# Performance work log

Measured on AMD Instinct MI355X. Metric: run time of the kernel, lower is better.

Reference implementation:

```python
import jax, jax.numpy as jnp
import numpy as np
import math

B, T, D, H = 4, 2048, 1024, 16
DH = D // H


def setup_inputs() -> dict:
    key = jax.random.key(0)
    k1, k2, k3 = jax.random.split(key, 3)
    x = jax.random.normal(k1, (B, T, D), dtype=jnp.float32)
    # causal mask: True = masked (positions j > i)
    attn_mask = jnp.triu(jnp.ones((T, T), dtype=bool), k=1)
    key_padding_mask = jnp.zeros((B, T), dtype=bool)  # no padding
    W_qkv = jax.random.normal(k2, (D, 3 * D), dtype=jnp.float32) / math.sqrt(D)
    W_out = jax.random.normal(k3, (D, D), dtype=jnp.float32) / math.sqrt(D)
    return {"x": x, "W_qkv": W_qkv, "W_out": W_out,
            "attn_mask": attn_mask, "key_padding_mask": key_padding_mask}


def reference(x, W_qkv, W_out, attn_mask, key_padding_mask):
    # qkv projection (bias=False)
    qkv = x @ W_qkv                                   # [B,T,3D]
    q, k, v = jnp.split(qkv, 3, axis=-1)              # each [B,T,D]
    # reshape to heads: [B,H,T,DH]
    q = q.reshape(B, T, H, DH).transpose(0, 2, 1, 3)
    k = k.reshape(B, T, H, DH).transpose(0, 2, 1, 3)
    v = v.reshape(B, T, H, DH).transpose(0, 2, 1, 3)
    scale = 1.0 / math.sqrt(DH)
    scores = jnp.einsum('bhqd,bhkd->bhqk', q, k) * scale   # [B,H,T,T]
    neg_inf = jnp.float32(-jnp.inf)
    scores = jnp.where(attn_mask[None, None, :, :], neg_inf, scores)
    scores = jnp.where(key_padding_mask[:, None, None, :], neg_inf, scores)
    attn = jax.nn.softmax(scores, axis=-1)            # dropout p=0.0 -> identity
    out = jnp.einsum('bhqk,bhkd->bhqd', attn, v)      # [B,H,T,DH]
    out = out.transpose(0, 2, 1, 3).reshape(B, T, D)
    return out @ W_out
```

## Files before the change

### kernel.cpp

```cpp
#include <hip/hip_runtime.h>
#include <hip/hip_bf16.h>

#define Bsz 4
#define T 2048
#define D 1024
#define H 16
#define DH 64

typedef unsigned short u16;
typedef __attribute__((ext_vector_type(8))) __bf16 bf16x8;
typedef __attribute__((ext_vector_type(4))) float f32x4;

__device__ inline u16 f2bf(float f) {
  union { float f; unsigned u; } v; v.f = f;
  unsigned r = (v.u + 0x7FFFu + ((v.u >> 16) & 1u)) >> 16;
  return (u16)r;
}
__device__ inline unsigned pack_bf16(float a, float b) {
  union { float f; unsigned u; } A, B; A.f = a; B.f = b;
  unsigned au = A.u + 0x8000u, bu = B.u + 0x8000u;
  return __builtin_amdgcn_perm(bu, au, 0x07060302);
}

__device__ inline void gll16(const u16* g, u16* l) {
  __builtin_amdgcn_global_load_lds((const __attribute__((address_space(1))) void*)g,
                                   (__attribute__((address_space(3))) void*)l, 16, 0, 0);
}

__global__ __launch_bounds__(256) void convert_f32_bf16(const float* __restrict__ in,
                                                        u16* __restrict__ out, int n4) {
  int i = blockIdx.x * 256 + threadIdx.x;
  if (i < n4) {
    float4 v = reinterpret_cast<const float4*>(in)[i];
    ushort4 o;
    o.x = f2bf(v.x); o.y = f2bf(v.y); o.z = f2bf(v.z); o.w = f2bf(v.w);
    reinterpret_cast<ushort4*>(out)[i] = o;
  }
}

__global__ __launch_bounds__(256) void transpose_f32_bf16(const float* __restrict__ in,
                                                          u16* __restrict__ out, int K, int N) {
  __shared__ float tile[32][33];
  int tx = threadIdx.x & 31, ty = threadIdx.x >> 5;
  int n0 = blockIdx.x * 32, k0 = blockIdx.y * 32;
  #pragma unroll
  for (int i = 0; i < 4; ++i)
    tile[ty + i * 8][tx] = in[(size_t)(k0 + ty + i * 8) * N + n0 + tx];
  __syncthreads();
  #pragma unroll
  for (int i = 0; i < 4; ++i)
    out[(size_t)(n0 + ty + i * 8) * K + k0 + tx] = f2bf(tile[tx][ty + i * 8]);
}

template <int MODE>
__global__ __launch_bounds__(512, 2) void gemm256(const u16* __restrict__ A, const u16* __restrict__ BT,
                                                  float* __restrict__ C,
                                                  u16* __restrict__ Qh, u16* __restrict__ Kh,
                                                  u16* __restrict__ VTh, int M, int N, int K) {
  __shared__ alignas(16) u16 SA[2][256][64];
  __shared__ alignas(16) u16 SB[2][256][64];
  int tid = threadIdx.x;

  int flat = blockIdx.y * gridDim.x + blockIdx.x;
  int cpx = (int)(gridDim.x * gridDim.y) >> 3;
  int nf = (flat & 7) * cpx + (flat >> 3);
  int bx = nf % (int)gridDim.x, by = nf / (int)gridDim.x;
  int m0 = by * 256, n0 = bx * 256;

  int w = tid >> 6, lane = tid & 63;
  int llo = lane & 15, lhi = lane >> 4;
  int wr = w >> 2, wc = w & 3;

  int cs0 = ((lhi ^ (llo & 7)) << 3);
  int cs1 = (((4 + lhi) ^ (llo & 7)) << 3);

  int srcCol = (((lane & 7) ^ ((lane >> 3) & 7)) << 3);
  const u16* gAl = A + (size_t)(m0 + w * 8 + (lane >> 3)) * K + srcCol;
  const u16* gBl = BT + (size_t)(n0 + w * 8 + (lane >> 3)) * K + srcCol;

  f32x4 acc[8][4];
  #pragma unroll
  for (int i = 0; i < 8; ++i)
    #pragma unroll
    for (int j = 0; j < 4; ++j) acc[i][j] = (f32x4){0.f, 0.f, 0.f, 0.f};

  int nt = K >> 6;

  auto stA = [&](int buf, int h, int c, int kt) {
    gll16(gAl + (h * 128 + c * 64) * K + kt * 64, &SA[buf][h * 128 + c * 64 + w * 8][0]);
  };
  auto stB = [&](int buf, int h, int c, int kt) {
    gll16(gBl + (h * 128 + c * 64) * K + kt * 64, &SB[buf][h * 128 + c * 64 + w * 8][0]);
  };

  stA(0, 0, 0, 0); stA(0, 0, 1, 0); stA(0, 1, 0, 0); stA(0, 1, 1, 0);
  stB(0, 0, 0, 0); stB(0, 0, 1, 0); stB(0, 1, 0, 0); stB(0, 1, 1, 0);
  stB(1, 0, 0, 1); stB(1, 0, 1, 1);
  stA(1, 0, 0, 1); stA(1, 0, 1, 1);
  asm volatile("s_waitcnt vmcnt(4)" ::: "memory");
  __builtin_amdgcn_s_barrier();
  __builtin_amdgcn_sched_barrier(0);

  bf16x8 aA[4][2], bB[4][2];

  #pragma unroll 2
  for (int t = 0; t < nt; ++t) {
    int p = t & 1;

    #pragma unroll
    for (int i = 0; i < 4; ++i) {
      aA[i][0] = *reinterpret_cast<const bf16x8*>(&SA[p][wr * 128 + i * 16 + llo][cs0]);
      aA[i][1] = *reinterpret_cast<const bf16x8*>(&SA[p][wr * 128 + i * 16 + llo][cs1]);
    }
    #pragma unroll
    for (int j = 0; j < 2; ++j) {
      bB[j][0] = *reinterpret_cast<const bf16x8*>(&SB[p][wc * 64 + j * 16 + llo][cs0]);
      bB[j][1] = *reinterpret_cast<const bf16x8*>(&SB[p][wc * 64 + j * 16 + llo][cs1]);
    }
    if (t + 1 < nt) { stA(1 - p, 1, 0, t + 1); stA(1 - p, 1, 1, t + 1); }
    __builtin_amdgcn_s_barrier();
    asm volatile("s_waitcnt lgkmcnt(0)" ::: "memory");
    __builtin_amdgcn_sched_barrier(0);
    __builtin_amdgcn_s_setprio(1);
    #pragma unroll
    for (int i = 0; i < 4; ++i)
      #pragma unroll
      for (int j = 0; j < 2; ++j) {
        acc[i][j] = __builtin_amdgcn_mfma_f32_16x16x32_bf16(aA[i][0], bB[j][0], acc[i][j], 0, 0, 0);
        acc[i][j] = __builtin_amdgcn_mfma_f32_16x16x32_bf16(aA[i][1], bB[j][1], acc[i][j], 0, 0, 0);
      }
    __builtin_amdgcn_s_setprio(0);
    __builtin_amdgcn_s_barrier();
    __builtin_amdgcn_sched_barrier(0);

    #pragma unroll
    for (int j = 2; j < 4; ++j) {
      bB[j][0] = *reinterpret_cast<const bf16x8*>(&SB[p][wc * 64 + j * 16 + llo][cs0]);
      bB[j][1] = *reinterpret_cast<const bf16x8*>(&SB[p][wc * 64 + j * 16 + llo][cs1]);
    }
    if (t + 1 < nt) { stB(1 - p, 1, 0, t + 1); stB(1 - p, 1, 1, t + 1); }
    __builtin_amdgcn_s_barrier();
    asm volatile("s_waitcnt lgkmcnt(0)" ::: "memory");
    __builtin_amdgcn_sched_barrier(0);
    __builtin_amdgcn_s_setprio(1);
    #pragma unroll
    for (int i = 0; i < 4; ++i)
      #pragma unroll
      for (int j = 2; j < 4; ++j) {
        acc[i][j] = __builtin_amdgcn_mfma_f32_16x16x32_bf16(aA[i][0], bB[j][0], acc[i][j], 0, 0, 0);
        acc[i][j] = __builtin_amdgcn_mfma_f32_16x16x32_bf16(aA[i][1], bB[j][1], acc[i][j], 0, 0, 0);
      }
    __builtin_amdgcn_s_setprio(0);
    __builtin_amdgcn_s_barrier();
    __builtin_amdgcn_sched_barrier(0);

    #pragma unroll
    for (int i = 0; i < 4; ++i) {
      aA[i][0] = *reinterpret_cast<const bf16x8*>(&SA[p][wr * 128 + 64 + i * 16 + llo][cs0]);
      aA[i][1] = *reinterpret_cast<const bf16x8*>(&SA[p][wr * 128 + 64 + i * 16 + llo][cs1]);
    }
    if (t + 2 < nt) { stB(p, 0, 0, t + 2); stB(p, 0, 1, t + 2); }
    __builtin_amdgcn_s_barrier();
    asm volatile("s_waitcnt lgkmcnt(0)" ::: "memory");
    __builtin_amdgcn_sched_barrier(0);
    __builtin_amdgcn_s_setprio(1);
    #pragma unroll
    for (int i = 0; i < 4; ++i)
      #pragma unroll
      for (int j = 0; j < 2; ++j) {
        acc[4 + i][j] = __builtin_amdgcn_mfma_f32_16x16x32_bf16(aA[i][0], bB[j][0], acc[4 + i][j], 0, 0, 0);
        acc[4 + i][j] = __builtin_amdgcn_mfma_f32_16x16x32_bf16(aA[i][1], bB[j][1], acc[4 + i][j], 0, 0, 0);
      }
    __builtin_amdgcn_s_setprio(0);
    __builtin_amdgcn_s_barrier();
    __builtin_amdgcn_sched_barrier(0);

    if (t + 2 < nt) { stA(p, 0, 0, t + 2); stA(p, 0, 1, t + 2); }
    __builtin_amdgcn_s_setprio(1);
    #pragma unroll
    for (int i = 0; i < 4; ++i)
      #pragma unroll
      for (int j = 2; j < 4; ++j) {
        acc[4 + i][j] = __builtin_amdgcn_mfma_f32_16x16x32_bf16(aA[i][0], bB[j][0], acc[4 + i][j], 0, 0, 0);
        acc[4 + i][j] = __builtin_amdgcn_mfma_f32_16x16x32_bf16(aA[i][1], bB[j][1], acc[4 + i][j], 0, 0, 0);
      }
    __builtin_amdgcn_s_setprio(0);
    if (t + 2 < nt)      asm volatile("s_waitcnt vmcnt(4)" ::: "memory");
    else if (t + 1 < nt) asm volatile("s_waitcnt vmcnt(0)" ::: "memory");
    __builtin_amdgcn_s_barrier();
    __builtin_amdgcn_sched_barrier(0);
  }

  if (MODE == 0) {
    #pragma unroll
    for (int i = 0; i < 8; ++i) {
      int ml = m0 + wr * 128 + i * 16 + lhi * 4;
      #pragma unroll
      for (int j = 0; j < 4; ++j) {
        int nl = n0 + wc * 64 + j * 16 + llo;
        #pragma unroll
        for (int r = 0; r < 4; ++r)
          C[(size_t)(ml + r) * N + nl] = acc[i][j][r];
      }
    }
  } else {
    int seg = n0 >> 10;
    #pragma unroll
    for (int i = 0; i < 8; ++i) {
      int mbase = m0 + wr * 128 + i * 16 + lhi * 4;
      int t0 = mbase & (T - 1);
      int b_ = mbase >> 11;
      #pragma unroll
      for (int j = 0; j < 4; ++j) {
        int nl = n0 + wc * 64 + j * 16 + llo;
        int h = (nl >> 6) & 15, d = nl & 63;
        int bh = b_ * H + h;
        if (seg == 0) {
          #pragma unroll
          for (int r = 0; r < 4; ++r)
            Qh[((size_t)bh * T + t0 + r) * DH + d] = f2bf(acc[i][j][r] * 0.125f);
        } else if (seg == 1) {
          #pragma unroll
          for (int r = 0; r < 4; ++r)
            Kh[((size_t)bh * T + t0 + r) * DH + d] = f2bf(acc[i][j][r]);
        } else {
          uint2 p;
          p.x = pack_bf16(acc[i][j][0], acc[i][j][1]);
          p.y = pack_bf16(acc[i][j][2], acc[i][j][3]);
          *reinterpret_cast<uint2*>(&VTh[((size_t)bh * DH + d) * T + t0]) = p;
        }
      }
    }
  }
}

template <int MODE>
__global__ __launch_bounds__(256) void gemm128(const u16* __restrict__ A, const u16* __restrict__ BT,
                                               float* __restrict__ C,
                                               u16* __restrict__ Qh, u16* __restrict__ Kh,
                                               u16* __restrict__ VTh, int M, int N, int K) {
  __shared__ u16 As[128][32];
  __shared__ u16 Bs[128][32];
  int tid = threadIdx.x;
  int m0 = blockIdx.y * 128, n0 = blockIdx.x * 128;
  int w = tid >> 6, lane = tid & 63;
  int llo = lane & 15, lhi = lane >> 4;
  int wm = (w >> 1) * 64, wn = (w & 1) * 64;

  f32x4 acc[4][4];
  #pragma unroll
  for (int i = 0; i < 4; ++i)
    #pragma unroll
    for (int j = 0; j < 4; ++j) acc[i][j] = (f32x4){0.f, 0.f, 0.f, 0.f};

  const u16* gA = A + (size_t)(m0 + w * 32 + (lane >> 2)) * K + (lane & 3) * 8;
  const u16* gB = BT + (size_t)(n0 + w * 32 + (lane >> 2)) * K + (lane & 3) * 8;

  for (int k0 = 0; k0 < K; k0 += 32) {
    gll16(gA + k0, &As[w * 32][0]);
    gll16(gA + (size_t)16 * K + k0, &As[w * 32 + 16][0]);
    gll16(gB + k0, &Bs[w * 32][0]);
    gll16(gB + (size_t)16 * K + k0, &Bs[w * 32 + 16][0]);
    __syncthreads();
    bf16x8 af[4], bfr[4];
    #pragma unroll
    for (int i = 0; i < 4; ++i)
      af[i] = *reinterpret_cast<const bf16x8*>(&As[wm + i * 16 + llo][lhi * 8]);
    #pragma unroll
    for (int j = 0; j < 4; ++j)
      bfr[j] = *reinterpret_cast<const bf16x8*>(&Bs[wn + j * 16 + llo][lhi * 8]);
    #pragma unroll
    for (int i = 0; i < 4; ++i)
      #pragma unroll
      for (int j = 0; j < 4; ++j)
        acc[i][j] = __builtin_amdgcn_mfma_f32_16x16x32_bf16(af[i], bfr[j], acc[i][j], 0, 0, 0);
    __syncthreads();
  }

  if (MODE == 0) {
    #pragma unroll
    for (int i = 0; i < 4; ++i)
      #pragma unroll
      for (int j = 0; j < 4; ++j) {
        int nl = n0 + wn + j * 16 + llo;
        #pragma unroll
        for (int r = 0; r < 4; ++r) {
          int ml = m0 + wm + i * 16 + lhi * 4 + r;
          C[(size_t)ml * N + nl] = acc[i][j][r];
        }
      }
  }
}

__global__ __launch_bounds__(1024, 4) void attn_fwd(const u16* __restrict__ Qh, const u16* __restrict__ Kh,
                                                    const u16* __restrict__ VTh, u16* __restrict__ AO) {
  __shared__ u16 QP[16][16][72];
  __shared__ u16 Ks[64][72];
  __shared__ u16 Vs[64][72];
  int tid = threadIdx.x;
  int qp = blockIdx.x, bh = blockIdx.y;
  int w = tid >> 6, lane = tid & 63;
  int llo = lane & 15, lhi = lane >> 4;

  int qrow_s = tid >> 2, qc = tid & 3;
  int krow_s = tid >> 4, kc = tid & 15;
  const u16* kbase = Kh + ((size_t)bh * T + krow_s) * DH + kc * 4;
  const u16* vbase = VTh + ((size_t)bh * DH + krow_s) * T + kc * 4;
  int b = bh >> 4, h = bh & 15;

  #pragma unroll 1
  for (int half = 0; half < 2; ++half) {
    int qt = half ? (7 - qp) : qp;
    int q0 = qt * 256;

    bf16x8 aq[2];
    {
      const uint4* g = reinterpret_cast<const uint4*>(
          Qh + ((size_t)bh * T + q0 + qrow_s) * DH + qc * 16);
      uint4 a = g[0], bb = g[1];
      uint4* dst = reinterpret_cast<uint4*>(&QP[w][qrow_s & 15][qc * 16]);
      dst[0] = a; dst[1] = bb;
      #pragma unroll
      for (int ks = 0; ks < 2; ++ks)
        aq[ks] = *reinterpret_cast<const bf16x8*>(&QP[w][llo][ks * 32 + lhi * 8]);
    }

    f32x4 o[4];
    #pragma unroll
    for (int i = 0; i < 4; ++i) o[i] = (f32x4){0.f, 0.f, 0.f, 0.f};
    float l_run = 0.f;

    int nj = 4 * qt + 4;
    uint2 ka = *reinterpret_cast<const uint2*>(kbase);
    uint2 va = *reinterpret_cast<const uint2*>(vbase);

    #pragma unroll 1
    for (int j = 0; j < nj; ++j) {
      __syncthreads();
      *reinterpret_cast<uint2*>(&Ks[krow_s][kc * 4]) = ka;
      *reinterpret_cast<uint2*>(&Vs[krow_s][kc * 4]) = va;
      if (j + 1 < nj) {
        ka = *reinterpret_cast<const uint2*>(kbase + (size_t)(j + 1) * 64 * DH);
        va = *reinterpret_cast<const uint2*>(vbase + (j + 1) * 64);
      } else if (half == 0) {
        ka = *reinterpret_cast<const uint2*>(kbase);
        va = *reinterpret_cast<const uint2*>(vbase);
      }
      __syncthreads();

      if (q0 + w * 16 + 15 >= j * 64) {
        f32x4 sc[4];
        #pragma unroll
        for (int kt = 0; kt < 4; ++kt) {
          bf16x8 bk0 = *reinterpret_cast<const bf16x8*>(&Ks[kt * 16 + llo][lhi * 8]);
          bf16x8 bk1 = *reinterpret_cast<const bf16x8*>(&Ks[kt * 16 + llo][32 + lhi * 8]);
          f32x4 z = (f32x4){0.f, 0.f, 0.f, 0.f};
          f32x4 t0 = __builtin_amdgcn_mfma_f32_16x16x32_bf16(bk0, aq[0], z, 0, 0, 0);
          sc[kt] = __builtin_amdgcn_mfma_f32_16x16x32_bf16(bk1, aq[1], t0, 0, 0, 0);
        }

        if (j >= 4 * qt) {
          int qrow_g = q0 + w * 16 + llo;
          #pragma unroll
          for (int kt = 0; kt < 4; ++kt)
            #pragma unroll
            for (int r = 0; r < 4; ++r) {
              int key_g = j * 64 + kt * 16 + lhi * 4 + r;
              if (key_g > qrow_g) sc[kt][r] = -__builtin_inff();
            }
        }

        float s_sum = 0.f;
        #pragma unroll
        for (int kt = 0; kt < 4; ++kt)
          #pragma unroll
          for (int r = 0; r < 4; ++r) {
            float p = __expf(sc[kt][r]);
            sc[kt][r] = p;
            s_sum += p;
          }
        s_sum += __shfl_xor(s_sum, 16);
        s_sum += __shfl_xor(s_sum, 32);
        l_run += s_sum;

        #pragma unroll
        for (int kt = 0; kt < 4; ++kt) {
          uint2 p;
          p.x = pack_bf16(sc[kt][0], sc[kt][1]);
          p.y = pack_bf16(sc[kt][2], sc[kt][3]);
          *reinterpret_cast<uint2*>(&QP[w][llo][kt * 16 + lhi * 4]) = p;
        }

        #pragma unroll
        for (int kk2 = 0; kk2 < 2; ++kk2) {
          bf16x8 pa = *reinterpret_cast<const bf16x8*>(&QP[w][llo][kk2 * 32 + lhi * 8]);
          #pragma unroll
          for (int nt = 0; nt < 4; ++nt) {
            bf16x8 bv = *reinterpret_cast<const bf16x8*>(&Vs[nt * 16 + llo][kk2 * 32 + lhi * 8]);
            o[nt] = __builtin_amdgcn_mfma_f32_16x16x32_bf16(pa, bv, o[nt], 0, 0, 0);
          }
        }
      }
    }

    #pragma unroll
    for (int r = 0; r < 4; ++r) {
      float inv = 1.f / __shfl(l_run, lhi * 4 + r);
      int t = q0 + w * 16 + lhi * 4 + r;
      #pragma unroll
      for (int nt = 0; nt < 4; ++nt)
        AO[((size_t)(b * T + t)) * D + h * 64 + nt * 16 + llo] = f2bf(o[nt][r] * inv);
    }
  }
}

extern "C" void kernel_launch(void* const* d_in, const int* in_sizes, int n_in,
                              void* d_out, int out_size, void* d_ws, size_t ws_size,
                              hipStream_t stream) {
  (void)in_sizes; (void)n_in; (void)out_size;
  const float* x = (const float*)d_in[0];
  const float* Wqkv = (const float*)d_in[1];
  const float* Wout = (const float*)d_in[2];
  float* out = (float*)d_out;

  char* ws = (char*)d_ws;
  size_t off = 0;
  u16* xb = (u16*)(ws + off);    off += (size_t)Bsz * T * D * 2;
  u16* WqkvT = (u16*)(ws + off); off += (size_t)3 * D * D * 2;
  u16* WoutT = (u16*)(ws + off); off += (size_t)D * D * 2;
  u16* Qh = (u16*)(ws + off);    off += (size_t)Bsz * H * T * DH * 2;
  u16* Kh = (u16*)(ws + off);    off += (size_t)Bsz * H * T * DH * 2;
  u16* VTh = (u16*)(ws + off);   off += (size_t)Bsz * H * DH * T * 2;
  u16* AO = xb;
  if (ws_size < off) return;

  int n4 = Bsz * T * D / 4;
  convert_f32_bf16<<<(n4 + 255) / 256, 256, 0, stream>>>(x, xb, n4);
  transpose_f32_bf16<<<dim3(3 * D / 32, D / 32), 256, 0, stream>>>(Wqkv, WqkvT, D, 3 * D);
  transpose_f32_bf16<<<dim3(D / 32, D / 32), 256, 0, stream>>>(Wout, WoutT, D, D);
  gemm256<1><<<dim3(3 * D / 256, Bsz * T / 256), 512, 0, stream>>>(xb, WqkvT, nullptr, Qh, Kh, VTh,
                                                                   Bsz * T, 3 * D, D);
  attn_fwd<<<dim3(4, Bsz * H), 1024, 0, stream>>>(Qh, Kh, VTh, AO);
  gemm128<0><<<dim3(D / 128, Bsz * T / 128), 256, 0, stream>>>(AO, WoutT, out, nullptr, nullptr, nullptr,
                                                               Bsz * T, D, D);
}
```

Baseline: 277.9 us.

## Use 256x192 tiles in QKV GEMM with reworked load pipeline

Changes the QKV projection GEMM tile from 256x256 to 256x192. This gives 16x32=512 blocks instead of 12x32=384, for better wave balance across CUs. The global-to-LDS prefetch schedule is reorganised into a simple one-step-ahead double buffer with new vmcnt waits. The Q/K/V segment is now computed per sub-tile, because a tile can straddle the Q/K/V boundaries. This costs lower arithmetic intensity per tile and a shallower prefetch, which may expose more memory latency.

```diff
diff --git a/kernel.cpp b/kernel.cpp
--- a/kernel.cpp
+++ b/kernel.cpp
@@ -58,14 +58,14 @@
                                                   u16* __restrict__ Qh, u16* __restrict__ Kh,
                                                   u16* __restrict__ VTh, int M, int N, int K) {
   __shared__ alignas(16) u16 SA[2][256][64];
-  __shared__ alignas(16) u16 SB[2][256][64];
+  __shared__ alignas(16) u16 SB[2][192][64];
   int tid = threadIdx.x;
 
   int flat = blockIdx.y * gridDim.x + blockIdx.x;
   int cpx = (int)(gridDim.x * gridDim.y) >> 3;
   int nf = (flat & 7) * cpx + (flat >> 3);
   int bx = nf % (int)gridDim.x, by = nf / (int)gridDim.x;
-  int m0 = by * 256, n0 = bx * 256;
+  int m0 = by * 256, n0 = bx * 192;
 
   int w = tid >> 6, lane = tid & 63;
   int llo = lane & 15, lhi = lane >> 4;
@@ -78,30 +78,28 @@
   const u16* gAl = A + (size_t)(m0 + w * 8 + (lane >> 3)) * K + srcCol;
   const u16* gBl = BT + (size_t)(n0 + w * 8 + (lane >> 3)) * K + srcCol;
 
-  f32x4 acc[8][4];
+  f32x4 acc[8][3];
   #pragma unroll
   for (int i = 0; i < 8; ++i)
     #pragma unroll
-    for (int j = 0; j < 4; ++j) acc[i][j] = (f32x4){0.f, 0.f, 0.f, 0.f};
+    for (int j = 0; j < 3; ++j) acc[i][j] = (f32x4){0.f, 0.f, 0.f, 0.f};
 
   int nt = K >> 6;
 
-  auto stA = [&](int buf, int h, int c, int kt) {
-    gll16(gAl + (h * 128 + c * 64) * K + kt * 64, &SA[buf][h * 128 + c * 64 + w * 8][0]);
+  auto stA = [&](int buf, int c, int kt) {
+    gll16(gAl + (size_t)(c * 64) * K + kt * 64, &SA[buf][c * 64 + w * 8][0]);
   };
-  auto stB = [&](int buf, int h, int c, int kt) {
-    gll16(gBl + (h * 128 + c * 64) * K + kt * 64, &SB[buf][h * 128 + c * 64 + w * 8][0]);
+  auto stB = [&](int buf, int c, int kt) {
+    gll16(gBl + (size_t)(c * 64) * K + kt * 64, &SB[buf][c * 64 + w * 8][0]);
   };
 
-  stA(0, 0, 0, 0); stA(0, 0, 1, 0); stA(0, 1, 0, 0); stA(0, 1, 1, 0);
-  stB(0, 0, 0, 0); stB(0, 0, 1, 0); stB(0, 1, 0, 0); stB(0, 1, 1, 0);
-  stB(1, 0, 0, 1); stB(1, 0, 1, 1);
-  stA(1, 0, 0, 1); stA(1, 0, 1, 1);
-  asm volatile("s_waitcnt vmcnt(4)" ::: "memory");
+  stA(0, 0, 0); stA(0, 1, 0); stA(0, 2, 0); stA(0, 3, 0);
+  stB(0, 0, 0); stB(0, 1, 0); stB(0, 2, 0);
+  asm volatile("s_waitcnt vmcnt(0)" ::: "memory");
   __builtin_amdgcn_s_barrier();
   __builtin_amdgcn_sched_barrier(0);
 
-  bf16x8 aA[4][2], bB[4][2];
+  bf16x8 aA[4][2], bB[3][2];
 
   #pragma unroll 2
   for (int t = 0; t < nt; ++t) {
@@ -114,10 +112,10 @@
     }
     #pragma unroll
     for (int j = 0; j < 2; ++j) {
-      bB[j][0] = *reinterpret_cast<const bf16x8*>(&SB[p][wc * 64 + j * 16 + llo][cs0]);
-      bB[j][1] = *reinterpret_cast<const bf16x8*>(&SB[p][wc * 64 + j * 16 + llo][cs1]);
-    }
-    if (t + 1 < nt) { stA(1 - p, 1, 0, t + 1); stA(1 - p, 1, 1, t + 1); }
+      bB[j][0] = *reinterpret_cast<const bf16x8*>(&SB[p][wc * 48 + j * 16 + llo][cs0]);
+      bB[j][1] = *reinterpret_cast<const bf16x8*>(&SB[p][wc * 48 + j * 16 + llo][cs1]);
+    }
+    if (t + 1 < nt) { stA(1 - p, 0, t + 1); stA(1 - p, 2, t + 1); }
     __builtin_amdgcn_s_barrier();
     asm volatile("s_waitcnt lgkmcnt(0)" ::: "memory");
     __builtin_amdgcn_sched_barrier(0);
@@ -133,24 +131,21 @@
     __builtin_amdgcn_s_barrier();
     __builtin_amdgcn_sched_barrier(0);
 
-    #pragma unroll
-    for (int j = 2; j < 4; ++j) {
-      bB[j][0] = *reinterpret_cast<const bf16x8*>(&SB[p][wc * 64 + j * 16 + llo][cs0]);
-      bB[j][1] = *reinterpret_cast<const bf16x8*>(&SB[p][wc * 64 + j * 16 + llo][cs1]);
-    }
-    if (t + 1 < nt) { stB(1 - p, 1, 0, t + 1); stB(1 - p, 1, 1, t + 1); }
+    bB[2][0] = *reinterpret_cast<const bf16x8*>(&SB[p][wc * 48 + 32 + llo][cs0]);
+    bB[2][1] = *reinterpret_cast<const bf16x8*>(&SB[p][wc * 48 + 32 + llo][cs1]);
+    if (t + 1 < nt) { stB(1 - p, 0, t + 1); stB(1 - p, 1, t + 1); }
     __builtin_amdgcn_s_barrier();
     asm volatile("s_waitcnt lgkmcnt(0)" ::: "memory");
     __builtin_amdgcn_sched_barrier(0);
     __builtin_amdgcn_s_setprio(1);
     #pragma unroll
-    for (int i = 0; i < 4; ++i)
-      #pragma unroll
-      for (int j = 2; j < 4; ++j) {
-        acc[i][j] = __builtin_amdgcn_mfma_f32_16x16x32_bf16(aA[i][0], bB[j][0], acc[i][j], 0, 0, 0);
-        acc[i][j] = __builtin_amdgcn_mfma_f32_16x16x32_bf16(aA[i][1], bB[j][1], acc[i][j], 0, 0, 0);
-      }
+    for (int i = 0; i < 4; ++i) {
+      acc[i][2] = __builtin_amdgcn_mfma_f32_16x16x32_bf16(aA[i][0], bB[2][0], acc[i][2], 0, 0, 0);
+      acc[i][2] = __builtin_amdgcn_mfma_f32_16x16x32_bf16(aA[i][1], bB[2][1], acc[i][2], 0, 0, 0);
+    }
     __builtin_amdgcn_s_setprio(0);
+    if (t + 1 < nt) asm volatile("s_waitcnt vmcnt(4)" ::: "memory");
+    else            asm volatile("s_waitcnt vmcnt(0)" ::: "memory");
     __builtin_amdgcn_s_barrier();
     __builtin_amdgcn_sched_barrier(0);
 
@@ -159,7 +154,7 @@
       aA[i][0] = *reinterpret_cast<const bf16x8*>(&SA[p][wr * 128 + 64 + i * 16 + llo][cs0]);
       aA[i][1] = *reinterpret_cast<const bf16x8*>(&SA[p][wr * 128 + 64 + i * 16 + llo][cs1]);
     }
-    if (t + 2 < nt) { stB(p, 0, 0, t + 2); stB(p, 0, 1, t + 2); }
+    if (t + 1 < nt) { stB(1 - p, 2, t + 1); stA(1 - p, 1, t + 1); }
     __builtin_amdgcn_s_barrier();
     asm volatile("s_waitcnt lgkmcnt(0)" ::: "memory");
     __builtin_amdgcn_sched_barrier(0);
@@ -175,18 +170,15 @@
     __builtin_amdgcn_s_barrier();
     __builtin_amdgcn_sched_barrier(0);
 
-    if (t + 2 < nt) { stA(p, 0, 0, t + 2); stA(p, 0, 1, t + 2); }
+    if (t + 1 < nt) stA(1 - p, 3, t + 1);
     __builtin_amdgcn_s_setprio(1);
     #pragma unroll
-    for (int i = 0; i < 4; ++i)
-      #pragma unroll
-      for (int j = 2; j < 4; ++j) {
-        acc[4 + i][j] = __builtin_amdgcn_mfma_f32_16x16x32_bf16(aA[i][0], bB[j][0], acc[4 + i][j], 0, 0, 0);
-        acc[4 + i][j] = __builtin_amdgcn_mfma_f32_16x16x32_bf16(aA[i][1], bB[j][1], acc[4 + i][j], 0, 0, 0);
-      }
+    for (int i = 0; i < 4; ++i) {
+      acc[4 + i][2] = __builtin_amdgcn_mfma_f32_16x16x32_bf16(aA[i][0], bB[2][0], acc[4 + i][2], 0, 0, 0);
+      acc[4 + i][2] = __builtin_amdgcn_mfma_f32_16x16x32_bf16(aA[i][1], bB[2][1], acc[4 + i][2], 0, 0, 0);
+    }
     __builtin_amdgcn_s_setprio(0);
-    if (t + 2 < nt)      asm volatile("s_waitcnt vmcnt(4)" ::: "memory");
-    else if (t + 1 < nt) asm volatile("s_waitcnt vmcnt(0)" ::: "memory");
+    if (t + 1 < nt) asm volatile("s_waitcnt vmcnt(2)" ::: "memory");
     __builtin_amdgcn_s_barrier();
     __builtin_amdgcn_sched_barrier(0);
   }
@@ -196,23 +188,23 @@
     for (int i = 0; i < 8; ++i) {
       int ml = m0 + wr * 128 + i * 16 + lhi * 4;
       #pragma unroll
-      for (int j = 0; j < 4; ++j) {
-        int nl = n0 + wc * 64 + j * 16 + llo;
+      for (int j = 0; j < 3; ++j) {
+        int nl = n0 + wc * 48 + j * 16 + llo;
         #pragma unroll
         for (int r = 0; r < 4; ++r)
           C[(size_t)(ml + r) * N + nl] = acc[i][j][r];
       }
     }
   } else {
-    int seg = n0 >> 10;
     #pragma unroll
     for (int i = 0; i < 8; ++i) {
       int mbase = m0 + wr * 128 + i * 16 + lhi * 4;
       int t0 = mbase & (T - 1);
       int b_ = mbase >> 11;
       #pragma unroll
-      for (int j = 0; j < 4; ++j) {
-        int nl = n0 + wc * 64 + j * 16 + llo;
+      for (int j = 0; j < 3; ++j) {
+        int nl = n0 + wc * 48 + j * 16 + llo;
+        int seg = (n0 + wc * 48 + j * 16) >> 10;
         int h = (nl >> 6) & 15, d = nl & 63;
         int bh = b_ * H + h;
         if (seg == 0) {
@@ -438,7 +430,7 @@
   convert_f32_bf16<<<(n4 + 255) / 256, 256, 0, stream>>>(x, xb, n4);
   transpose_f32_bf16<<<dim3(3 * D / 32, D / 32), 256, 0, stream>>>(Wqkv, WqkvT, D, 3 * D);
   transpose_f32_bf16<<<dim3(D / 32, D / 32), 256, 0, stream>>>(Wout, WoutT, D, D);
-  gemm256<1><<<dim3(3 * D / 256, Bsz * T / 256), 512, 0, stream>>>(xb, WqkvT, nullptr, Qh, Kh, VTh,
+  gemm256<1><<<dim3(3 * D / 192, Bsz * T / 256), 512, 0, stream>>>(xb, WqkvT, nullptr, Qh, Kh, VTh,
                                                                    Bsz * T, 3 * D, D);
   attn_fwd<<<dim3(4, Bsz * H), 1024, 0, stream>>>(Qh, Kh, VTh, AO);
   gemm128<0><<<dim3(D / 128, Bsz * T / 128), 256, 0, stream>>>(AO, WoutT, out, nullptr, nullptr, nullptr,
```

Result: faster. 271.9 us (-2.1%).
